# Optimization experiments

Measured on AMD Instinct MI355X. Metric: run time of the kernel, lower is better.

Reference implementation:

```python
import jax, jax.numpy as jnp
import numpy as np

N_NODES = 100000


def setup_inputs() -> dict:
    key = jax.random.key(0)
    k1, k2, k3, k4 = jax.random.split(key, 4)
    E = 1600000
    in_dim, out_dim = 256, 64
    h = jax.random.normal(k1, (N_NODES, in_dim), dtype=jnp.float32)
    src = jax.random.randint(k2, (E,), 0, N_NODES, dtype=jnp.int64)
    dst = jax.random.randint(k3, (E,), 0, N_NODES, dtype=jnp.int64)
    W = jax.random.normal(k4, (in_dim, out_dim), dtype=jnp.float32) * (1.0 / np.sqrt(in_dim))
    b = jnp.zeros((out_dim,), dtype=jnp.float32)
    return {"h": h, "src": src, "dst": dst, "W": W, "b": b}


def reference(h, src, dst, W, b):
    # dgl GraphConv, norm='both': out = D_in^{-1/2} A D_out^{-1/2} h W + b
    E = src.shape[0]
    ones = jnp.ones((E,), dtype=h.dtype)
    deg_out = jax.ops.segment_sum(ones, src, num_segments=N_NODES)  # out-degree of src nodes
    deg_in = jax.ops.segment_sum(ones, dst, num_segments=N_NODES)   # in-degree of dst nodes
    norm_src = jnp.clip(deg_out, 1.0, None) ** -0.5                  # [N]
    norm_dst = jnp.clip(deg_in, 1.0, None) ** -0.5                   # [N]
    # in_dim > out_dim: project first (as dgl does), then aggregate small features
    x = (h * norm_src[:, None]) @ W                                  # [N, out_dim]
    msgs = x[src]                                                    # [E, out_dim] gather
    agg = jax.ops.segment_sum(msgs, dst, num_segments=N_NODES)      # [N, out_dim] scatter-add
    out = agg * norm_dst[:, None] + b
    # ReLU; dropout is identity in eval mode
    return jax.nn.relu(out)
```

## Files before the change

kernel.cpp:

```cpp
#include <hip/hip_runtime.h>
#include <hip/hip_fp16.h>

#define N_NODES 100000
#define IN_DIM 256
#define OUT_DIM 64
#define NT 782
#define NSC 512
#define SMAX 3200
#define CAP_F 3072

typedef _Float16 half8 __attribute__((ext_vector_type(8)));
typedef float f32x4 __attribute__((ext_vector_type(4)));

__global__ __launch_bounds__(256) void init_kernel(int* __restrict__ cursorD,
                                                   int* __restrict__ cursorS) {
    for (int i = threadIdx.x; i < NT; i += 256) { cursorD[i] = 0; cursorS[i] = 0; }
}

__global__ __launch_bounds__(256) void scatter_kernel(const int* __restrict__ src,
                                                      const int* __restrict__ dst,
                                                      int* __restrict__ cursorD,
                                                      int* __restrict__ cursorS,
                                                      int* __restrict__ binnedD,
                                                      unsigned char* __restrict__ srcb,
                                                      int E, int chunk) {
    __shared__ int sorted[SMAX];
    __shared__ unsigned short sbin[SMAX];
    __shared__ unsigned char sortedB[SMAX];
    __shared__ unsigned short sbinS[SMAX];
    __shared__ int histD[NT], boffD[NT], resvD[NT];
    __shared__ int histS[NT], boffS[NT], resvS[NT];
    const int t = threadIdx.x, blk = blockIdx.x;
    const int lane = t & 63, wv = t >> 6;
    const int lo = blk * chunk;
    int hiA = lo + chunk; if (hiA > E) hiA = E;
    for (int s0 = lo; s0 < hiA; s0 += SMAX) {
        int m = hiA - s0; if (m > SMAX) m = SMAX;
        for (int i = t; i < NT; i += 256) { histD[i] = 0; histS[i] = 0; }
        __syncthreads();
        for (int k = t; k < m; k += 256) {
            int s = src[s0 + k], d = dst[s0 + k];
            atomicAdd(&histD[d >> 7], 1);
            atomicAdd(&histS[s >> 7], 1);
        }
        __syncthreads();
        if (wv < 2) {
            int* hsrc = (wv == 0) ? histD : histS;
            int* bdst = (wv == 0) ? boffD : boffS;
            int carry = 0;
            for (int r = 0; r < (NT + 63) / 64; ++r) {
                int i = r * 64 + lane;
                int v = (i < NT) ? hsrc[i] : 0;
                int incl = v;
#pragma unroll
                for (int off = 1; off < 64; off <<= 1) {
                    int y = __shfl_up(incl, off);
                    if (lane >= off) incl += y;
                }
                if (i < NT) bdst[i] = carry + incl - v;
                carry += __shfl(incl, 63);
            }
        }
        __syncthreads();
        for (int i = t; i < NT; i += 256) {
            int hd = histD[i];
            if (hd) resvD[i] = atomicAdd(&cursorD[i], hd);
            int hs = histS[i];
            if (hs) resvS[i] = atomicAdd(&cursorS[i], hs);
            histD[i] = boffD[i];
            histS[i] = boffS[i];
        }
        __syncthreads();
        for (int k = t; k < m; k += 256) {
            int s = src[s0 + k], d = dst[s0 + k];
            int bd = d >> 7;
            int p = atomicAdd(&histD[bd], 1);
            sorted[p] = (s << 7) | (d & 127);
            sbin[p] = (unsigned short)bd;
            int bs = s >> 7;
            int ps = atomicAdd(&histS[bs], 1);
            sortedB[ps] = (unsigned char)(s & 127);
            sbinS[ps] = (unsigned short)bs;
        }
        __syncthreads();
        for (int k = t; k < m; k += 256) {
            int b = sbin[k];
            int loc = resvD[b] + (k - boffD[b]);
            if (loc < CAP_F) binnedD[b * CAP_F + loc] = sorted[k];
            int bs = sbinS[k];
            int locS = resvS[bs] + (k - boffS[bs]);
            if (locS < CAP_F) srcb[bs * CAP_F + locS] = sortedB[k];
        }
        __syncthreads();
    }
}

__global__ __launch_bounds__(256) void tile_kernel(const int* __restrict__ cursorD,
                                                   const int* __restrict__ cursorS,
                                                   const int* __restrict__ binnedD,
                                                   const unsigned char* __restrict__ srcb,
                                                   int* __restrict__ csr,
                                                   int* __restrict__ offs, int* __restrict__ cnt,
                                                   int* __restrict__ deg_out) {
    __shared__ int h[128], cur[128];
    __shared__ int lcsr[CAP_F];
    __shared__ int w0tot;
    const int bin = blockIdx.x, t = threadIdx.x, lane = t & 63;
    if (t < 128) h[t] = 0;
    __syncthreads();

    const int base = bin * CAP_F;
    int m = cursorD[bin]; if (m > CAP_F) m = CAP_F;
    for (int k = t; k < m; k += 256) atomicAdd(&h[binnedD[base + k] & 127], 1);
    __syncthreads();
    int v = (t < 128) ? h[t] : 0;
    int incl = v;
#pragma unroll
    for (int off = 1; off < 64; off <<= 1) {
        int y = __shfl_up(incl, off);
        if (lane >= off) incl += y;
    }
    if (t == 63) w0tot = incl;
    __syncthreads();
    int excl = incl - v + ((t >= 64 && t < 128) ? w0tot : 0);
    if (t < 128) {
        cur[t] = excl;
        int node = bin * 128 + t;
        if (node < N_NODES) { offs[node] = base + excl; cnt[node] = v; }
    }
    __syncthreads();
    for (int k = t; k < m; k += 256) {
        int rec = binnedD[base + k];
        int p = atomicAdd(&cur[rec & 127], 1);
        lcsr[p] = rec >> 7;
    }
    __syncthreads();
    for (int k = t; k < m; k += 256) csr[base + k] = lcsr[k];

    __syncthreads();
    if (t < 128) h[t] = 0;
    __syncthreads();
    int ms = cursorS[bin]; if (ms > CAP_F) ms = CAP_F;
    const int sbase = bin * CAP_F;
    for (int k = t; k < ms; k += 256) atomicAdd(&h[srcb[sbase + k]], 1);
    __syncthreads();
    if (t < 128) {
        int node = bin * 128 + t;
        if (node < N_NODES) deg_out[node] = h[t];
    }
}

#define A_LD 136
__global__ __launch_bounds__(256) void gemm_kernel(const float* __restrict__ hmat,
                                                   const float* __restrict__ W,
                                                   const int* __restrict__ deg_out,
                                                   __half* __restrict__ xh) {
    __shared__ _Float16 sA[64 * A_LD];
    __shared__ _Float16 sB[64 * A_LD];
    const int t = threadIdx.x;
    const int lane = t & 63;
    const int w = t >> 6;
    const int row0 = blockIdx.x * 64;
    const int m0 = (w & 1) * 32;
    const int n0 = (w >> 1) * 32;

    f32x4 acc00 = {0.f, 0.f, 0.f, 0.f}, acc01 = {0.f, 0.f, 0.f, 0.f};
    f32x4 acc10 = {0.f, 0.f, 0.f, 0.f}, acc11 = {0.f, 0.f, 0.f, 0.f};

    for (int khalf = 0; khalf < 2; ++khalf) {
        const int k0 = khalf * 128;
        __syncthreads();
#pragma unroll
        for (int it = 0; it < 8; ++it) {
            int f = t + it * 256;
            int row = f >> 5;
            int c4 = f & 31;
            int grow = row0 + row; if (grow >= N_NODES) grow = N_NODES - 1;
            float4 v = *(const float4*)(hmat + (size_t)grow * IN_DIM + k0 + c4 * 4);
            _Float16 p[4];
            p[0] = (_Float16)v.x; p[1] = (_Float16)v.y;
            p[2] = (_Float16)v.z; p[3] = (_Float16)v.w;
            *(uint2*)&sA[row * A_LD + c4 * 4] = *(uint2*)p;
        }
        {
            int n = t & 63;
            int kk0 = (t >> 6) * 32;
#pragma unroll
            for (int kb = 0; kb < 8; ++kb) {
                _Float16 p[4];
#pragma unroll
                for (int u = 0; u < 4; ++u)
                    p[u] = (_Float16)W[(size_t)(k0 + kk0 + kb * 4 + u) * OUT_DIM + n];
                *(uint2*)&sB[n * A_LD + kk0 + kb * 4] = *(uint2*)p;
            }
        }
        __syncthreads();
#pragma unroll
        for (int kb = 0; kb < 4; ++kb) {
            int koff = kb * 32 + (lane >> 4) * 8;
            half8 a0 = *(const half8*)&sA[(m0 + (lane & 15)) * A_LD + koff];
            half8 a1 = *(const half8*)&sA[(m0 + 16 + (lane & 15)) * A_LD + koff];
            half8 b0 = *(const half8*)&sB[(n0 + (lane & 15)) * A_LD + koff];
            half8 b1 = *(const half8*)&sB[(n0 + 16 + (lane & 15)) * A_LD + koff];
            acc00 = __builtin_amdgcn_mfma_f32_16x16x32_f16(a0, b0, acc00, 0, 0, 0);
            acc01 = __builtin_amdgcn_mfma_f32_16x16x32_f16(a0, b1, acc01, 0, 0, 0);
            acc10 = __builtin_amdgcn_mfma_f32_16x16x32_f16(a1, b0, acc10, 0, 0, 0);
            acc11 = __builtin_amdgcn_mfma_f32_16x16x32_f16(a1, b1, acc11, 0, 0, 0);
        }
    }

    const int col16 = lane & 15;
    const int rq = (lane >> 4) * 4;
#pragma unroll
    for (int mi = 0; mi < 2; ++mi) {
        float nrm[4];
#pragma unroll
        for (int r = 0; r < 4; ++r) {
            int row = row0 + m0 + mi * 16 + rq + r;
            int d = (row < N_NODES) ? deg_out[row] : 1;
            nrm[r] = rsqrtf((float)(d < 1 ? 1 : d));
        }
#pragma unroll
        for (int ni = 0; ni < 2; ++ni) {
            const f32x4 a = (mi == 0) ? (ni == 0 ? acc00 : acc01)
                                      : (ni == 0 ? acc10 : acc11);
            int col = n0 + ni * 16 + col16;
#pragma unroll
            for (int r = 0; r < 4; ++r) {
                int row = row0 + m0 + mi * 16 + rq + r;
                if (row < N_NODES)
                    xh[(size_t)row * OUT_DIM + col] = __float2half(a[r] * nrm[r]);
            }
        }
    }
}

__global__ __launch_bounds__(256) void aggregate_kernel(const int* __restrict__ offs,
                                                        const int* __restrict__ cnt,
                                                        const int* __restrict__ csr,
                                                        const __half* __restrict__ xh,
                                                        const float* __restrict__ b,
                                                        float* __restrict__ out) {
    const int t = threadIdx.x;
    const int lane = t & 63;
    const int wid = t >> 6;
    const int node = blockIdx.x * 4 + wid;
    const int g = lane >> 3;
    const int c = lane & 7;

    const int start = offs[node];
    const int n = cnt[node];

    float acc[8] = {0.f, 0.f, 0.f, 0.f, 0.f, 0.f, 0.f, 0.f};
    for (int base = 0; base < n; base += 64) {
        int k = base + lane;
        int sidx = (k < n) ? csr[start + k] : 0;
        int m = n - base; if (m > 64) m = 64;
        for (int e0 = 0; e0 < m; e0 += 16) {
            int ea = e0 + g;
            int eb = e0 + 8 + g;
            int sa = __shfl(sidx, ea);
            int sb = __shfl(sidx, eb);
            bool va = ea < m;
            bool vb = eb < m;
            float wa = va ? 1.f : 0.f;
            float wb = vb ? 1.f : 0.f;
            uint4 ra = *(const uint4*)(xh + (size_t)(va ? sa : 0) * OUT_DIM + 8 * c);
            const bool grpb = (e0 + 8) < m;
            uint4 rb;
            if (grpb)
                rb = *(const uint4*)(xh + (size_t)(vb ? sb : 0) * OUT_DIM + 8 * c);
            {
                const __half2* hp = (const __half2*)&ra;
#pragma unroll
                for (int p = 0; p < 4; ++p) {
                    float2 f = __half22float2(hp[p]);
                    acc[2 * p]     = fmaf(wa, f.x, acc[2 * p]);
                    acc[2 * p + 1] = fmaf(wa, f.y, acc[2 * p + 1]);
                }
            }
            if (grpb) {
                const __half2* hp = (const __half2*)&rb;
#pragma unroll
                for (int p = 0; p < 4; ++p) {
                    float2 f = __half22float2(hp[p]);
                    acc[2 * p]     = fmaf(wb, f.x, acc[2 * p]);
                    acc[2 * p + 1] = fmaf(wb, f.y, acc[2 * p + 1]);
                }
            }
        }
    }

#pragma unroll
    for (int off = 8; off < 64; off <<= 1) {
#pragma unroll
        for (int p = 0; p < 8; ++p)
            acc[p] += __shfl_xor(acc[p], off);
    }

    if (g == 0) {
        float nrm = rsqrtf((float)(n < 1 ? 1 : n));
        float4 bv0 = *(const float4*)&b[c * 8];
        float4 bv1 = *(const float4*)&b[c * 8 + 4];
        float4 r0, r1;
        r0.x = fmaxf(fmaf(acc[0], nrm, bv0.x), 0.f);
        r0.y = fmaxf(fmaf(acc[1], nrm, bv0.y), 0.f);
        r0.z = fmaxf(fmaf(acc[2], nrm, bv0.z), 0.f);
        r0.w = fmaxf(fmaf(acc[3], nrm, bv0.w), 0.f);
        r1.x = fmaxf(fmaf(acc[4], nrm, bv1.x), 0.f);
        r1.y = fmaxf(fmaf(acc[5], nrm, bv1.y), 0.f);
        r1.z = fmaxf(fmaf(acc[6], nrm, bv1.z), 0.f);
        r1.w = fmaxf(fmaf(acc[7], nrm, bv1.w), 0.f);
        float4* orow = (float4*)(out + (size_t)node * OUT_DIM + c * 8);
        orow[0] = r0;
        orow[1] = r1;
    }
}

extern "C" void kernel_launch(void* const* d_in, const int* in_sizes, int n_in,
                              void* d_out, int out_size, void* d_ws, size_t ws_size,
                              hipStream_t stream) {
    const float* h   = (const float*)d_in[0];
    const int*   src = (const int*)d_in[1];
    const int*   dst = (const int*)d_in[2];
    const float* W   = (const float*)d_in[3];
    const float* b   = (const float*)d_in[4];
    float* out = (float*)d_out;
    const int E = in_sizes[1];
    const int chunkS = (E + NSC - 1) / NSC;

    char* ws = (char*)d_ws;
    int*           cursorD = (int*)(ws);
    int*           cursorS = (int*)(ws + 3328);
    int*           binnedD = (int*)(ws + 6656);
    int*           csr     = binnedD;
    unsigned char* srcb    = (unsigned char*)(ws + 9615872);
    int*           offs    = (int*)(ws + 12018176);
    int*           cntA    = (int*)(ws + 12418176);
    int*           deg_out = (int*)(ws + 12818176);
    __half*        xh      = (__half*)(ws + 13218176);

    init_kernel<<<1, 256, 0, stream>>>(cursorD, cursorS);
    scatter_kernel<<<NSC, 256, 0, stream>>>(src, dst, cursorD, cursorS, binnedD, srcb, E, chunkS);
    tile_kernel<<<NT, 256, 0, stream>>>(cursorD, cursorS, binnedD, srcb, csr, offs, cntA, deg_out);
    gemm_kernel<<<(N_NODES + 63) / 64, 256, 0, stream>>>(h, W, deg_out, xh);
    aggregate_kernel<<<N_NODES / 4, 256, 0, stream>>>(offs, cntA, csr, xh, b, out);
}
```

Before: 263.5 us.

## Run GEMM concurrently with edge binning and apply source norm in aggregation

Merges the edge-scatter binning and the feature projection GEMM into one launch, with block IDs split between the two roles, so the bandwidth-heavy GEMM over h overlaps the atomic-heavy scatter. To remove the GEMM's dependence on out-degree, the source normalisation moves out of the GEMM epilogue. The tile kernel now writes per-node rsqrt norms, and the aggregation multiplies each gathered row by its source norm. This costs one extra scalar gather per edge in aggregation and uses a larger shared-memory footprint for the fused kernel, which may lower occupancy of the GEMM blocks.

Result: faster. 253.6 us (-3.7%).

```diff
diff --git a/kernel.cpp b/kernel.cpp
--- a/kernel.cpp
+++ b/kernel.cpp
@@ -8,90 +8,175 @@
 #define NSC 512
 #define SMAX 3200
 #define CAP_F 3072
+#define GEMM_BLKS 1563
 
 typedef _Float16 half8 __attribute__((ext_vector_type(8)));
 typedef float f32x4 __attribute__((ext_vector_type(4)));
 
 __global__ __launch_bounds__(256) void init_kernel(int* __restrict__ cursorD,
                                                    int* __restrict__ cursorS) {
-    for (int i = threadIdx.x; i < NT; i += 256) { cursorD[i] = 0; cursorS[i] = 0; }
-}
-
-__global__ __launch_bounds__(256) void scatter_kernel(const int* __restrict__ src,
-                                                      const int* __restrict__ dst,
-                                                      int* __restrict__ cursorD,
-                                                      int* __restrict__ cursorS,
-                                                      int* __restrict__ binnedD,
-                                                      unsigned char* __restrict__ srcb,
-                                                      int E, int chunk) {
-    __shared__ int sorted[SMAX];
-    __shared__ unsigned short sbin[SMAX];
-    __shared__ unsigned char sortedB[SMAX];
-    __shared__ unsigned short sbinS[SMAX];
-    __shared__ int histD[NT], boffD[NT], resvD[NT];
-    __shared__ int histS[NT], boffS[NT], resvS[NT];
-    const int t = threadIdx.x, blk = blockIdx.x;
-    const int lane = t & 63, wv = t >> 6;
-    const int lo = blk * chunk;
-    int hiA = lo + chunk; if (hiA > E) hiA = E;
-    for (int s0 = lo; s0 < hiA; s0 += SMAX) {
-        int m = hiA - s0; if (m > SMAX) m = SMAX;
-        for (int i = t; i < NT; i += 256) { histD[i] = 0; histS[i] = 0; }
-        __syncthreads();
-        for (int k = t; k < m; k += 256) {
-            int s = src[s0 + k], d = dst[s0 + k];
-            atomicAdd(&histD[d >> 7], 1);
-            atomicAdd(&histS[s >> 7], 1);
-        }
-        __syncthreads();
-        if (wv < 2) {
-            int* hsrc = (wv == 0) ? histD : histS;
-            int* bdst = (wv == 0) ? boffD : boffS;
-            int carry = 0;
-            for (int r = 0; r < (NT + 63) / 64; ++r) {
-                int i = r * 64 + lane;
-                int v = (i < NT) ? hsrc[i] : 0;
-                int incl = v;
-#pragma unroll
-                for (int off = 1; off < 64; off <<= 1) {
-                    int y = __shfl_up(incl, off);
-                    if (lane >= off) incl += y;
-                }
-                if (i < NT) bdst[i] = carry + incl - v;
-                carry += __shfl(incl, 63);
-            }
-        }
-        __syncthreads();
-        for (int i = t; i < NT; i += 256) {
-            int hd = histD[i];
-            if (hd) resvD[i] = atomicAdd(&cursorD[i], hd);
-            int hs = histS[i];
-            if (hs) resvS[i] = atomicAdd(&cursorS[i], hs);
-            histD[i] = boffD[i];
-            histS[i] = boffS[i];
-        }
-        __syncthreads();
-        for (int k = t; k < m; k += 256) {
-            int s = src[s0 + k], d = dst[s0 + k];
-            int bd = d >> 7;
-            int p = atomicAdd(&histD[bd], 1);
-            sorted[p] = (s << 7) | (d & 127);
-            sbin[p] = (unsigned short)bd;
-            int bs = s >> 7;
-            int ps = atomicAdd(&histS[bs], 1);
-            sortedB[ps] = (unsigned char)(s & 127);
-            sbinS[ps] = (unsigned short)bs;
-        }
-        __syncthreads();
-        for (int k = t; k < m; k += 256) {
-            int b = sbin[k];
-            int loc = resvD[b] + (k - boffD[b]);
-            if (loc < CAP_F) binnedD[b * CAP_F + loc] = sorted[k];
-            int bs = sbinS[k];
-            int locS = resvS[bs] + (k - boffS[bs]);
-            if (locS < CAP_F) srcb[bs * CAP_F + locS] = sortedB[k];
-        }
-        __syncthreads();
+    int i = blockIdx.x * 256 + threadIdx.x;
+    if (i < NT) { cursorD[i] = 0; cursorS[i] = 0; }
+}
+
+#define A_LD 136
+__global__ __launch_bounds__(256) void fused_kernel(const int* __restrict__ src,
+                                                    const int* __restrict__ dst,
+                                                    int* __restrict__ cursorD,
+                                                    int* __restrict__ cursorS,
+                                                    int* __restrict__ binnedD,
+                                                    unsigned char* __restrict__ srcb,
+                                                    const float* __restrict__ hmat,
+                                                    const float* __restrict__ W,
+                                                    __half* __restrict__ xh,
+                                                    int E, int chunk) {
+    __shared__ char smem[47568];
+    const int t = threadIdx.x;
+    if (blockIdx.x < NSC) {
+        int* sorted            = (int*)(smem);
+        int* histD             = (int*)(smem + 12800);
+        int* boffD             = (int*)(smem + 15928);
+        int* resvD             = (int*)(smem + 19056);
+        int* histS             = (int*)(smem + 22184);
+        int* boffS             = (int*)(smem + 25312);
+        int* resvS             = (int*)(smem + 28440);
+        unsigned short* sbin   = (unsigned short*)(smem + 31568);
+        unsigned short* sbinS  = (unsigned short*)(smem + 37968);
+        unsigned char* sortedB = (unsigned char*)(smem + 44368);
+        const int blk = blockIdx.x;
+        const int lane = t & 63, wv = t >> 6;
+        const int lo = blk * chunk;
+        int hiA = lo + chunk; if (hiA > E) hiA = E;
+        for (int s0 = lo; s0 < hiA; s0 += SMAX) {
+            int m = hiA - s0; if (m > SMAX) m = SMAX;
+            for (int i = t; i < NT; i += 256) { histD[i] = 0; histS[i] = 0; }
+            __syncthreads();
+            for (int k = t; k < m; k += 256) {
+                int s = src[s0 + k], d = dst[s0 + k];
+                atomicAdd(&histD[d >> 7], 1);
+                atomicAdd(&histS[s >> 7], 1);
+            }
+            __syncthreads();
+            if (wv < 2) {
+                int* hsrc = (wv == 0) ? histD : histS;
+                int* bdst = (wv == 0) ? boffD : boffS;
+                int carry = 0;
+                for (int r = 0; r < (NT + 63) / 64; ++r) {
+                    int i = r * 64 + lane;
+                    int v = (i < NT) ? hsrc[i] : 0;
+                    int incl = v;
+#pragma unroll
+                    for (int off = 1; off < 64; off <<= 1) {
+                        int y = __shfl_up(incl, off);
+                        if (lane >= off) incl += y;
+                    }
+                    if (i < NT) bdst[i] = carry + incl - v;
+                    carry += __shfl(incl, 63);
+                }
+            }
+            __syncthreads();
+            for (int i = t; i < NT; i += 256) {
+                int hd = histD[i];
+                if (hd) resvD[i] = atomicAdd(&cursorD[i], hd);
+                int hs = histS[i];
+                if (hs) resvS[i] = atomicAdd(&cursorS[i], hs);
+                histD[i] = boffD[i];
+                histS[i] = boffS[i];
+            }
+            __syncthreads();
+            for (int k = t; k < m; k += 256) {
+                int s = src[s0 + k], d = dst[s0 + k];
+                int bd = d >> 7;
+                int p = atomicAdd(&histD[bd], 1);
+                sorted[p] = (s << 7) | (d & 127);
+                sbin[p] = (unsigned short)bd;
+                int bs = s >> 7;
+                int ps = atomicAdd(&histS[bs], 1);
+                sortedB[ps] = (unsigned char)(s & 127);
+                sbinS[ps] = (unsigned short)bs;
+            }
+            __syncthreads();
+            for (int k = t; k < m; k += 256) {
+                int b = sbin[k];
+                int loc = resvD[b] + (k - boffD[b]);
+                if (loc < CAP_F) binnedD[b * CAP_F + loc] = sorted[k];
+                int bs = sbinS[k];
+                int locS = resvS[bs] + (k - boffS[bs]);
+                if (locS < CAP_F) srcb[bs * CAP_F + locS] = sortedB[k];
+            }
+            __syncthreads();
+        }
+    } else {
+        _Float16* sA = (_Float16*)(smem);
+        _Float16* sB = (_Float16*)(smem + 64 * A_LD * 2);
+        const int lane = t & 63;
+        const int w = t >> 6;
+        const int row0 = (blockIdx.x - NSC) * 64;
+        const int m0 = (w & 1) * 32;
+        const int n0 = (w >> 1) * 32;
+
+        f32x4 acc00 = {0.f, 0.f, 0.f, 0.f}, acc01 = {0.f, 0.f, 0.f, 0.f};
+        f32x4 acc10 = {0.f, 0.f, 0.f, 0.f}, acc11 = {0.f, 0.f, 0.f, 0.f};
+
+        for (int khalf = 0; khalf < 2; ++khalf) {
+            const int k0 = khalf * 128;
+            __syncthreads();
+#pragma unroll
+            for (int it = 0; it < 8; ++it) {
+                int f = t + it * 256;
+                int row = f >> 5;
+                int c4 = f & 31;
+                int grow = row0 + row; if (grow >= N_NODES) grow = N_NODES - 1;
+                float4 v = *(const float4*)(hmat + (size_t)grow * IN_DIM + k0 + c4 * 4);
+                _Float16 p[4];
+                p[0] = (_Float16)v.x; p[1] = (_Float16)v.y;
+                p[2] = (_Float16)v.z; p[3] = (_Float16)v.w;
+                *(uint2*)&sA[row * A_LD + c4 * 4] = *(uint2*)p;
+            }
+            {
+                int n = t & 63;
+                int kk0 = (t >> 6) * 32;
+#pragma unroll
+                for (int kb = 0; kb < 8; ++kb) {
+                    _Float16 p[4];
+#pragma unroll
+                    for (int u = 0; u < 4; ++u)
+                        p[u] = (_Float16)W[(size_t)(k0 + kk0 + kb * 4 + u) * OUT_DIM + n];
+                    *(uint2*)&sB[n * A_LD + kk0 + kb * 4] = *(uint2*)p;
+                }
+            }
+            __syncthreads();
+#pragma unroll
+            for (int kb = 0; kb < 4; ++kb) {
+                int koff = kb * 32 + (lane >> 4) * 8;
+                half8 a0 = *(const half8*)&sA[(m0 + (lane & 15)) * A_LD + koff];
+                half8 a1 = *(const half8*)&sA[(m0 + 16 + (lane & 15)) * A_LD + koff];
+                half8 b0 = *(const half8*)&sB[(n0 + (lane & 15)) * A_LD + koff];
+                half8 b1 = *(const half8*)&sB[(n0 + 16 + (lane & 15)) * A_LD + koff];
+                acc00 = __builtin_amdgcn_mfma_f32_16x16x32_f16(a0, b0, acc00, 0, 0, 0);
+                acc01 = __builtin_amdgcn_mfma_f32_16x16x32_f16(a0, b1, acc01, 0, 0, 0);
+                acc10 = __builtin_amdgcn_mfma_f32_16x16x32_f16(a1, b0, acc10, 0, 0, 0);
+                acc11 = __builtin_amdgcn_mfma_f32_16x16x32_f16(a1, b1, acc11, 0, 0, 0);
+            }
+        }
+
+        const int col16 = lane & 15;
+        const int rq = (lane >> 4) * 4;
+#pragma unroll
+        for (int mi = 0; mi < 2; ++mi) {
+#pragma unroll
+            for (int ni = 0; ni < 2; ++ni) {
+                const f32x4 a = (mi == 0) ? (ni == 0 ? acc00 : acc01)
+                                          : (ni == 0 ? acc10 : acc11);
+                int col = n0 + ni * 16 + col16;
+#pragma unroll
+                for (int r = 0; r < 4; ++r) {
+                    int row = row0 + m0 + mi * 16 + rq + r;
+                    if (row < N_NODES)
+                        xh[(size_t)row * OUT_DIM + col] = __float2half(a[r]);
+                }
+            }
+        }
     }
 }
 
@@ -101,7 +186,7 @@
                                                    const unsigned char* __restrict__ srcb,
                                                    int* __restrict__ csr,
                                                    int* __restrict__ offs, int* __restrict__ cnt,
-                                                   int* __restrict__ deg_out) {
+                                                   float* __restrict__ nrmS) {
     __shared__ int h[128], cur[128];
     __shared__ int lcsr[CAP_F];
     __shared__ int w0tot;
@@ -146,91 +231,9 @@
     __syncthreads();
     if (t < 128) {
         int node = bin * 128 + t;
-        if (node < N_NODES) deg_out[node] = h[t];
-    }
-}
-
-#define A_LD 136
-__global__ __launch_bounds__(256) void gemm_kernel(const float* __restrict__ hmat,
-                                                   const float* __restrict__ W,
-                                                   const int* __restrict__ deg_out,
-                                                   __half* __restrict__ xh) {
-    __shared__ _Float16 sA[64 * A_LD];
-    __shared__ _Float16 sB[64 * A_LD];
-    const int t = threadIdx.x;
-    const int lane = t & 63;
-    const int w = t >> 6;
-    const int row0 = blockIdx.x * 64;
-    const int m0 = (w & 1) * 32;
-    const int n0 = (w >> 1) * 32;
-
-    f32x4 acc00 = {0.f, 0.f, 0.f, 0.f}, acc01 = {0.f, 0.f, 0.f, 0.f};
-    f32x4 acc10 = {0.f, 0.f, 0.f, 0.f}, acc11 = {0.f, 0.f, 0.f, 0.f};
-
-    for (int khalf = 0; khalf < 2; ++khalf) {
-        const int k0 = khalf * 128;
-        __syncthreads();
-#pragma unroll
-        for (int it = 0; it < 8; ++it) {
-            int f = t + it * 256;
-            int row = f >> 5;
-            int c4 = f & 31;
-            int grow = row0 + row; if (grow >= N_NODES) grow = N_NODES - 1;
-            float4 v = *(const float4*)(hmat + (size_t)grow * IN_DIM + k0 + c4 * 4);
-            _Float16 p[4];
-            p[0] = (_Float16)v.x; p[1] = (_Float16)v.y;
-            p[2] = (_Float16)v.z; p[3] = (_Float16)v.w;
-            *(uint2*)&sA[row * A_LD + c4 * 4] = *(uint2*)p;
-        }
-        {
-            int n = t & 63;
-            int kk0 = (t >> 6) * 32;
-#pragma unroll
-            for (int kb = 0; kb < 8; ++kb) {
-                _Float16 p[4];
-#pragma unroll
-                for (int u = 0; u < 4; ++u)
-                    p[u] = (_Float16)W[(size_t)(k0 + kk0 + kb * 4 + u) * OUT_DIM + n];
-                *(uint2*)&sB[n * A_LD + kk0 + kb * 4] = *(uint2*)p;
-            }
-        }
-        __syncthreads();
-#pragma unroll
-        for (int kb = 0; kb < 4; ++kb) {
-            int koff = kb * 32 + (lane >> 4) * 8;
-            half8 a0 = *(const half8*)&sA[(m0 + (lane & 15)) * A_LD + koff];
-            half8 a1 = *(const half8*)&sA[(m0 + 16 + (lane & 15)) * A_LD + koff];
-            half8 b0 = *(const half8*)&sB[(n0 + (lane & 15)) * A_LD + koff];
-            half8 b1 = *(const half8*)&sB[(n0 + 16 + (lane & 15)) * A_LD + koff];
-            acc00 = __builtin_amdgcn_mfma_f32_16x16x32_f16(a0, b0, acc00, 0, 0, 0);
-            acc01 = __builtin_amdgcn_mfma_f32_16x16x32_f16(a0, b1, acc01, 0, 0, 0);
-            acc10 = __builtin_amdgcn_mfma_f32_16x16x32_f16(a1, b0, acc10, 0, 0, 0);
-            acc11 = __builtin_amdgcn_mfma_f32_16x16x32_f16(a1, b1, acc11, 0, 0, 0);
-        }
-    }
-
-    const int col16 = lane & 15;
-    const int rq = (lane >> 4) * 4;
-#pragma unroll
-    for (int mi = 0; mi < 2; ++mi) {
-        float nrm[4];
-#pragma unroll
-        for (int r = 0; r < 4; ++r) {
-            int row = row0 + m0 + mi * 16 + rq + r;
-            int d = (row < N_NODES) ? deg_out[row] : 1;
-            nrm[r] = rsqrtf((float)(d < 1 ? 1 : d));
-        }
-#pragma unroll
-        for (int ni = 0; ni < 2; ++ni) {
-            const f32x4 a = (mi == 0) ? (ni == 0 ? acc00 : acc01)
-                                      : (ni == 0 ? acc10 : acc11);
-            int col = n0 + ni * 16 + col16;
-#pragma unroll
-            for (int r = 0; r < 4; ++r) {
-                int row = row0 + m0 + mi * 16 + rq + r;
-                if (row < N_NODES)
-                    xh[(size_t)row * OUT_DIM + col] = __float2half(a[r] * nrm[r]);
-            }
+        if (node < N_NODES) {
+            int d = h[t];
+            nrmS[node] = rsqrtf((float)(d < 1 ? 1 : d));
         }
     }
 }
@@ -238,6 +241,7 @@
 __global__ __launch_bounds__(256) void aggregate_kernel(const int* __restrict__ offs,
                                                         const int* __restrict__ cnt,
                                                         const int* __restrict__ csr,
+                                                        const float* __restrict__ nrmS,
                                                         const __half* __restrict__ xh,
                                                         const float* __restrict__ b,
                                                         float* __restrict__ out) {
@@ -263,13 +267,15 @@
             int sb = __shfl(sidx, eb);
             bool va = ea < m;
             bool vb = eb < m;
-            float wa = va ? 1.f : 0.f;
-            float wb = vb ? 1.f : 0.f;
+            float wa = va ? nrmS[sa] : 0.f;
             uint4 ra = *(const uint4*)(xh + (size_t)(va ? sa : 0) * OUT_DIM + 8 * c);
             const bool grpb = (e0 + 8) < m;
             uint4 rb;
-            if (grpb)
+            float wb = 0.f;
+            if (grpb) {
+                wb = vb ? nrmS[sb] : 0.f;
                 rb = *(const uint4*)(xh + (size_t)(vb ? sb : 0) * OUT_DIM + 8 * c);
+            }
             {
                 const __half2* hp = (const __half2*)&ra;
 #pragma unroll
@@ -337,12 +343,12 @@
     unsigned char* srcb    = (unsigned char*)(ws + 9615872);
     int*           offs    = (int*)(ws + 12018176);
     int*           cntA    = (int*)(ws + 12418176);
-    int*           deg_out = (int*)(ws + 12818176);
+    float*         nrmS    = (float*)(ws + 12818176);
     __half*        xh      = (__half*)(ws + 13218176);
 
-    init_kernel<<<1, 256, 0, stream>>>(cursorD, cursorS);
-    scatter_kernel<<<NSC, 256, 0, stream>>>(src, dst, cursorD, cursorS, binnedD, srcb, E, chunkS);
-    tile_kernel<<<NT, 256, 0, stream>>>(cursorD, cursorS, binnedD, srcb, csr, offs, cntA, deg_out);
-    gemm_kernel<<<(N_NODES + 63) / 64, 256, 0, stream>>>(h, W, deg_out, xh);
-    aggregate_kernel<<<N_NODES / 4, 256, 0, stream>>>(offs, cntA, csr, xh, b, out);
-}
+    init_kernel<<<4, 256, 0, stream>>>(cursorD, cursorS);
+    fused_kernel<<<NSC + GEMM_BLKS, 256, 0, stream>>>(src, dst, cursorD, cursorS,
+                                                      binnedD, srcb, h, W, xh, E, chunkS);
+    tile_kernel<<<NT, 256, 0, stream>>>(cursorD, cursorS, binnedD, srcb, csr, offs, cntA, nrmS);
+    aggregate_kernel<<<N_NODES / 4, 256, 0, stream>>>(offs, cntA, csr, nrmS, xh, b, out);
+}
```
